# Optimization experiments

Measured on AMD Instinct MI355X. Metric: run time of the kernel, lower is better.

The kernel has to match this reference:

```python
import jax, jax.numpy as jnp
import numpy as np

IMG = 224; P = 16; C = 3
G = IMG // P; N = G * G            # 14, 196 patches
DIM = 768; DEPTH = 6; HEADS = 12; DH = 64; MLP = 3072
INNER = HEADS * DH                  # 768
PD = C * P * P                      # 768 patch_dim
B = 32


def _coords():
    m, n = np.meshgrid(np.arange(G), np.arange(G))
    return jnp.asarray(np.stack((m, n), axis=-1).reshape(-1, 2), jnp.float32)  # (N,2)


def _ln(x, g, b, eps=1e-5):
    mu = jnp.mean(x, -1, keepdims=True)
    var = jnp.mean((x - mu) ** 2, -1, keepdims=True)
    return (x - mu) * jax.lax.rsqrt(var + eps) * g + b


def setup_inputs() -> dict:
    key = jax.random.key(0)
    ks = jax.random.split(key, 16)
    s = 0.02
    inp = {
        "img": jax.random.normal(ks[0], (B, C, IMG, IMG), jnp.float32),
        "noise_token": jnp.zeros((1,), jnp.float32),
        "A_noise": jax.random.normal(ks[1], (B, 2, 2), jnp.float32),
        "b_noise": jax.random.normal(ks[2], (B, 2), jnp.float32),
        "A_mean": jnp.eye(2, dtype=jnp.float32),
        "b_mean": jnp.zeros((2,), jnp.float32),
        "A_std": jnp.zeros((2, 2), jnp.float32),   # variance_init=0.0
        "b_std": jnp.zeros((2,), jnp.float32),
        "band_width": jnp.asarray(1.0, jnp.float32),
        "Wp": jax.random.normal(ks[3], (PD, DIM), jnp.float32) * s,
        "bp": jnp.zeros((DIM,), jnp.float32),
        "ln1_g": jnp.ones((DEPTH, DIM), jnp.float32),
        "ln1_b": jnp.zeros((DEPTH, DIM), jnp.float32),
        "Wqkv": jax.random.normal(ks[4], (DEPTH, DIM, 3 * INNER), jnp.float32) * s,
        "Wout": jax.random.normal(ks[5], (DEPTH, INNER, DIM), jnp.float32) * s,
        "bout": jnp.zeros((DEPTH, DIM), jnp.float32),
        "ln2_g": jnp.ones((DEPTH, DIM), jnp.float32),
        "ln2_b": jnp.zeros((DEPTH, DIM), jnp.float32),
        "Wff1": jax.random.normal(ks[6], (DEPTH, DIM, MLP), jnp.float32) * s,
        "bff1": jnp.zeros((DEPTH, MLP), jnp.float32),
        "Wff2": jax.random.normal(ks[7], (DEPTH, MLP, DIM), jnp.float32) * s,
        "bff2": jnp.zeros((DEPTH, DIM), jnp.float32),
        "Wep": jax.random.normal(ks[8], (DIM, PD), jnp.float32) * s,
        "bep": jnp.zeros((PD,), jnp.float32),
    }
    return inp


def reference(img, noise_token, A_noise, b_noise, A_mean, b_mean, A_std, b_std,
              band_width, Wp, bp, ln1_g, ln1_b, Wqkv, Wout, bout,
              ln2_g, ln2_b, Wff1, bff1, Wff2, bff2, Wep, bep):
    del noise_token  # deleted in the original forward
    b = img.shape[0]
    X = _coords()  # (N,2) base patch grid coords, non-trainable buffer
    # patchify: b c (h p1) (w p2) -> b (h w) (p1 p2 c)
    x = img.reshape(b, C, G, P, G, P).transpose(0, 2, 4, 3, 5, 1).reshape(b, N, PD)
    x = x @ Wp + bp
    # stochastic affine transform of coordinates
    A = A_mean + jax.nn.softplus(A_std) * A_noise          # (b,2,2)
    bt = b_mean + jax.nn.softplus(b_std) * b_noise         # (b,2)
    Xt = jnp.einsum('pd,bdo->bpo', X, A) + bt[:, None, :]  # (b,N,2)
    # RBF attention scores: dots[b,i,j] = -||Xt[b,j] - X[i]||^2 / band_width
    diff = Xt[:, None, :, :] - X[None, :, None, :]         # (b,N,N,2)
    dots = -jnp.sum(diff ** 2, axis=-1) / band_width       # (b,N,N)
    attn = jax.nn.softmax(dots, axis=-1)                   # same for all heads/layers
    for l in range(DEPTH):
        y = _ln(x, ln1_g[l], ln1_b[l])
        qkv = y @ Wqkv[l]                                  # q,k unused (pos_only=True)
        v = qkv[..., 2 * INNER:].reshape(b, N, HEADS, DH).transpose(0, 2, 1, 3)
        o = jnp.einsum('bij,bhjd->bhid', attn, v)
        o = o.transpose(0, 2, 1, 3).reshape(b, N, INNER)
        x = o @ Wout[l] + bout[l]                          # NOTE: no residual on attention (matches source)
        h = _ln(x, ln2_g[l], ln2_b[l])
        h = jax.nn.gelu(h @ Wff1[l] + bff1[l], approximate=False) @ Wff2[l] + bff2[l]
        x = x + h
    x = x @ Wep + bep
    # un-patchify: b (h w) (p1 p2 c) -> b c (h p1) (w p2)
    out = x.reshape(b, G, G, P, P, C).transpose(0, 5, 1, 3, 2, 4).reshape(b, C, IMG, IMG)
    return out
```

## Files before the change

### kernel.cpp

```cpp
#include <hip/hip_runtime.h>
#include <hip/hip_bf16.h>
#include <math.h>

#define NTOK 196
#define KPAD 224
#define BATCH 32
#define ROWS (BATCH * NTOK)
#define DIMC 768
#define MLPD 3072

typedef __hip_bfloat16 bf16;
typedef short bf16x8 __attribute__((ext_vector_type(8)));
typedef float f32x4 __attribute__((ext_vector_type(4)));

__device__ __forceinline__ void gload16(const void* g, void* l) {
    __builtin_amdgcn_global_load_lds(
        (__attribute__((address_space(1))) void*)const_cast<void*>(g),
        (__attribute__((address_space(3))) void*)l, 16, 0, 0);
}

__device__ __forceinline__ float softplus_f(float x) {
    return fmaxf(x, 0.f) + log1pf(expf(-fabsf(x)));
}
__device__ __forceinline__ float gelu_f(float x) {
    return 0.5f * x * (1.f + erff(x * 0.70710678118654752f));
}
__device__ __forceinline__ float to_f(float x) { return x; }
__device__ __forceinline__ float to_f(bf16 x) { return __bfloat162float(x); }

__global__ __launch_bounds__(64) void attn_kernel(
    const float* __restrict__ A_noise, const float* __restrict__ b_noise,
    const float* __restrict__ A_mean,  const float* __restrict__ b_mean,
    const float* __restrict__ A_std,   const float* __restrict__ b_std,
    const float* __restrict__ bwp, bf16* __restrict__ attn)
{
    int bi = blockIdx.x;
    int b = bi / NTOK, i = bi % NTOK;
    int lane = threadIdx.x;
    float A00 = A_mean[0] + softplus_f(A_std[0]) * A_noise[b * 4 + 0];
    float A01 = A_mean[1] + softplus_f(A_std[1]) * A_noise[b * 4 + 1];
    float A10 = A_mean[2] + softplus_f(A_std[2]) * A_noise[b * 4 + 2];
    float A11 = A_mean[3] + softplus_f(A_std[3]) * A_noise[b * 4 + 3];
    float bt0 = b_mean[0] + softplus_f(b_std[0]) * b_noise[b * 2 + 0];
    float bt1 = b_mean[1] + softplus_f(b_std[1]) * b_noise[b * 2 + 1];
    float inv_bw = 1.f / bwp[0];
    float Xi0 = (float)(i % 14), Xi1 = (float)(i / 14);
    float d[4];
    float mx = -1e30f;
    #pragma unroll
    for (int r = 0; r < 4; ++r) {
        int j = lane + r * 64;
        if (j < NTOK) {
            float Xj0 = (float)(j % 14), Xj1 = (float)(j / 14);
            float t0 = Xj0 * A00 + Xj1 * A10 + bt0 - Xi0;
            float t1 = Xj0 * A01 + Xj1 * A11 + bt1 - Xi1;
            d[r] = -(t0 * t0 + t1 * t1) * inv_bw;
            mx = fmaxf(mx, d[r]);
        } else d[r] = -1e30f;
    }
    for (int off = 1; off < 64; off <<= 1) mx = fmaxf(mx, __shfl_xor(mx, off));
    float e[4]; float s = 0.f;
    #pragma unroll
    for (int r = 0; r < 4; ++r) {
        int j = lane + r * 64;
        e[r] = (j < NTOK) ? expf(d[r] - mx) : 0.f;
        s += e[r];
    }
    for (int off = 1; off < 64; off <<= 1) s += __shfl_xor(s, off);
    float inv = 1.f / s;
    bf16* row = attn + (long)bi * KPAD;
    #pragma unroll
    for (int r = 0; r < 4; ++r) {
        int j = lane + r * 64;
        if (j < KPAD) row[j] = __float2bfloat16(j < NTOK ? e[r] * inv : 0.f);
    }
}

__global__ __launch_bounds__(256) void patchify_kernel(
    const float* __restrict__ img, bf16* __restrict__ Xp)
{
    long idx = (long)blockIdx.x * 256 + threadIdx.x;
    if (idx >= (long)ROWS * DIMC) return;
    int pd = (int)(idx % DIMC); long r = idx / DIMC;
    int n = (int)(r % NTOK); int b = (int)(r / NTOK);
    int c = pd % 3; int pp = pd / 3; int p2 = pp % 16; int p1 = pp / 16;
    int gw = n % 14, gh = n / 14;
    int h = gh * 16 + p1, w = gw * 16 + p2;
    Xp[idx] = __float2bfloat16(img[(((long)b * 3 + c) * 224 + h) * 224 + w]);
}

__global__ __launch_bounds__(256) void unpatchify_kernel(
    const float* __restrict__ xe, float* __restrict__ out)
{
    long idx = (long)blockIdx.x * 256 + threadIdx.x;
    if (idx >= (long)BATCH * 3 * 224 * 224) return;
    int w = (int)(idx % 224); long r = idx / 224;
    int h = (int)(r % 224); r /= 224;
    int c = (int)(r % 3); int b = (int)(r / 3);
    int gh = h / 16, p1 = h % 16, gw = w / 16, p2 = w % 16;
    int n = gh * 14 + gw;
    int pd = (p1 * 16 + p2) * 3 + c;
    out[idx] = xe[((long)b * NTOK + n) * DIMC + pd];
}

__global__ __launch_bounds__(256) void ln_kernel(
    const float* __restrict__ x, const float* __restrict__ g,
    const float* __restrict__ bb, bf16* __restrict__ y)
{
    int row = blockIdx.x;
    const float* xr = x + (long)row * DIMC;
    bf16* yr = y + (long)row * DIMC;
    int t = threadIdx.x;
    float v0 = xr[t], v1 = xr[t + 256], v2 = xr[t + 512];
    float s = v0 + v1 + v2;
    float s2 = v0 * v0 + v1 * v1 + v2 * v2;
    for (int off = 32; off; off >>= 1) { s += __shfl_down(s, off); s2 += __shfl_down(s2, off); }
    __shared__ float ps[4], ps2[4];
    if ((t & 63) == 0) { ps[t >> 6] = s; ps2[t >> 6] = s2; }
    __syncthreads();
    float S = ps[0] + ps[1] + ps[2] + ps[3];
    float S2 = ps2[0] + ps2[1] + ps2[2] + ps2[3];
    float mean = S * (1.f / DIMC);
    float var = S2 * (1.f / DIMC) - mean * mean;
    float rs = rsqrtf(var + 1e-5f);
    yr[t]       = __float2bfloat16((v0 - mean) * rs * g[t]       + bb[t]);
    yr[t + 256] = __float2bfloat16((v1 - mean) * rs * g[t + 256] + bb[t + 256]);
    yr[t + 512] = __float2bfloat16((v2 - mean) * rs * g[t + 512] + bb[t + 512]);
}

template<typename TIN>
__global__ __launch_bounds__(256) void transpose_cvt(
    const TIN* __restrict__ in, bf16* __restrict__ out,
    int R, int C, int ldin, int ldout, int Rpad, long sIn, long sOut)
{
    __shared__ float tile[32][33];
    in  += (long)blockIdx.z * sIn;
    out += (long)blockIdx.z * sOut;
    int c0 = blockIdx.x * 32, r0 = blockIdx.y * 32;
    int tx = threadIdx.x & 31, ty = threadIdx.x >> 5;
    #pragma unroll
    for (int i = 0; i < 32; i += 8) {
        int r = r0 + ty + i, c = c0 + tx;
        float v = 0.f;
        if (r < R && c < C) v = to_f(in[(long)r * ldin + c]);
        tile[ty + i][tx] = v;
    }
    __syncthreads();
    #pragma unroll
    for (int i = 0; i < 32; i += 8) {
        int c = c0 + ty + i, r = r0 + tx;
        if (c < C && r < Rpad) out[(long)c * ldout + r] = __float2bfloat16(tile[tx][ty + i]);
    }
}

__global__ __launch_bounds__(256) void cvt_kernel(const float* __restrict__ in,
                                                  bf16* __restrict__ out, int n)
{
    int i = blockIdx.x * 256 + threadIdx.x;
    if (i < n) out[i] = __float2bfloat16(in[i]);
}

__global__ __launch_bounds__(256) void cvt_wv_kernel(const float* __restrict__ Wqkv,
                                                     bf16* __restrict__ out)
{
    long i = (long)blockIdx.x * 256 + threadIdx.x;
    if (i >= 6L * 768 * 768) return;
    int c = (int)(i % 768); long rl = i / 768;
    int r = (int)(rl % 768); int l = (int)(rl / 768);
    out[i] = __float2bfloat16(Wqkv[((long)l * 768 + r) * 2304 + 1536 + c]);
}

template<int BN, int ACT, int ACCUM, int OUTF32, int GUARDM>
__global__ __launch_bounds__(256) void gemm_bf16(
    const bf16* __restrict__ A, const bf16* __restrict__ Bt,
    const float* __restrict__ bias, void* __restrict__ Cv,
    int M, int K, int lda, int ldb, int ldc,
    long sA, long sB, long sC)
{
    constexpr int FN = BN / 32;
    constexpr int LPT = 2 + BN / 64;
    constexpr int BSTRIDE = BN * 32;
    constexpr int SMEM = (BN == 128) ? 49152 : 36864;
    __shared__ __align__(16) char smem[SMEM];
    bf16* As = (bf16*)smem;
    bf16* Bs = (bf16*)(smem + 3 * 8192);
    A  += (long)blockIdx.z * sA;
    Bt += (long)blockIdx.z * sB;
    const int nwg = gridDim.x * gridDim.y;
    const int id = blockIdx.x + gridDim.x * blockIdx.y;
    const int q8 = nwg >> 3, r8 = nwg & 7;
    const int xcd = id & 7, jj = id >> 3;
    const int v = (xcd < r8 ? xcd * (q8 + 1) : r8 * (q8 + 1) + (xcd - r8) * q8) + jj;
    const int bx = v % gridDim.x, by = v / gridDim.x;
    const int m0 = by * 128, n0 = bx * BN;
    const int t = threadIdx.x, wave = t >> 6, lane = t & 63;
    const int lrow = t >> 2;
    const int lcol = ((t & 3) ^ ((lrow >> 1) & 3)) * 8;
    const bf16* ag = A  + (long)(m0 + lrow) * lda + lcol;
    const bf16* bg = Bt + (long)(n0 + lrow) * ldb + lcol;
    const int fr = lane & 15, kq = lane >> 4;
    const int swz = (fr >> 1) & 3;
    const int wr = wave >> 1, wc = wave & 1;
    f32x4 acc[4][FN];
    #pragma unroll
    for (int m = 0; m < 4; ++m)
        #pragma unroll
        for (int n = 0; n < FN; ++n) acc[m][n] = (f32x4){0.f, 0.f, 0.f, 0.f};

    auto stage = [&](int kt, int bufi) {
        const int k0 = kt << 5;
        bf16* ab = As + bufi * 4096 + wave * 512;
        bf16* bb = Bs + bufi * BSTRIDE + wave * 512;
        gload16(ag + k0, ab);
        gload16(ag + 64 * (long)lda + k0, ab + 2048);
        gload16(bg + k0, bb);
        if constexpr (BN == 128) gload16(bg + 64 * (long)ldb + k0, bb + 2048);
    };
    auto compute = [&](int bufi) {
        const bf16* as = As + bufi * 4096;
        const bf16* bs = Bs + bufi * BSTRIDE;
        bf16x8 af[4], bfv[FN];
        #pragma unroll
        for (int m = 0; m < 4; ++m)
            af[m] = *(const bf16x8*)&as[(wr * 64 + m * 16 + fr) * 32 + ((kq ^ swz) << 3)];
        #pragma unroll
        for (int n = 0; n < FN; ++n)
            bfv[n] = *(const bf16x8*)&bs[(wc * (BN / 2) + n * 16 + fr) * 32 + ((kq ^ swz) << 3)];
        __builtin_amdgcn_s_setprio(1);
        #pragma unroll
        for (int m = 0; m < 4; ++m)
            #pragma unroll
            for (int n = 0; n < FN; ++n)
                acc[m][n] = __builtin_amdgcn_mfma_f32_16x16x32_bf16(af[m], bfv[n], acc[m][n], 0, 0, 0);
        __builtin_amdgcn_s_setprio(0);
    };

    const int nt = K >> 5;
    stage(0, 0);
    stage(1, 1);
    int cur = 0, pf = 2;
    for (int it = 0; it < nt - 1; ++it) {
        asm volatile("s_waitcnt vmcnt(%0)" :: "n"(LPT) : "memory");
        __builtin_amdgcn_s_barrier();
        __builtin_amdgcn_sched_barrier(0);
        if (it + 2 < nt) stage(it + 2, pf);
        compute(cur);
        cur = (cur == 2) ? 0 : cur + 1;
        pf  = (pf  == 2) ? 0 : pf + 1;
    }
    asm volatile("s_waitcnt vmcnt(0)" ::: "memory");
    __builtin_amdgcn_s_barrier();
    __builtin_amdgcn_sched_barrier(0);
    compute(cur);
    __syncthreads();

    const int rbase = kq * 4;
    if constexpr (OUTF32) {
        static_assert(BN == 64, "f32 epilogue assumes BN=64");
        float* Cs = (float*)smem;
        #pragma unroll
        for (int n = 0; n < FN; ++n) {
            int lc = wc * (BN / 2) + n * 16 + fr;
            float bi = bias ? bias[n0 + lc] : 0.f;
            #pragma unroll
            for (int m = 0; m < 4; ++m)
                #pragma unroll
                for (int r = 0; r < 4; ++r) {
                    int lr = wr * 64 + m * 16 + rbase + r;
                    float vv = acc[m][n][r] + bi;
                    if (ACT) vv = gelu_f(vv);
                    Cs[lr * BN + lc] = vv;
                }
        }
        __syncthreads();
        float* Cp = (float*)Cv + (long)blockIdx.z * sC;
        #pragma unroll
        for (int i = 0; i < (128 * BN) / (256 * 4); ++i) {
            int chunk = i * 256 + t;
            int row = chunk / (BN / 4), c4 = (chunk % (BN / 4)) * 4;
            int gm = m0 + row;
            if (GUARDM && gm >= M) continue;
            float4 v4 = *(const float4*)&Cs[row * BN + c4];
            float* p = Cp + (long)gm * ldc + n0 + c4;
            if (ACCUM) {
                float4 o4 = *(const float4*)p;
                v4.x += o4.x; v4.y += o4.y; v4.z += o4.z; v4.w += o4.w;
            }
            *(float4*)p = v4;
        }
    } else {
        bf16* Cs = (bf16*)smem;
        #pragma unroll
        for (int n = 0; n < FN; ++n) {
            int lc = wc * (BN / 2) + n * 16 + fr;
            float bi = bias ? bias[n0 + lc] : 0.f;
            #pragma unroll
            for (int m = 0; m < 4; ++m)
                #pragma unroll
                for (int r = 0; r < 4; ++r) {
                    int lr = wr * 64 + m * 16 + rbase + r;
                    float vv = acc[m][n][r] + bi;
                    if (ACT) vv = gelu_f(vv);
                    Cs[lr * BN + lc] = __float2bfloat16(vv);
                }
        }
        __syncthreads();
        bf16* Cp = (bf16*)Cv + (long)blockIdx.z * sC;
        #pragma unroll
        for (int i = 0; i < (128 * BN) / (256 * 8); ++i) {
            int chunk = i * 256 + t;
            int row = chunk / (BN / 8), c8 = (chunk % (BN / 8)) * 8;
            int gm = m0 + row;
            if (GUARDM && gm >= M) continue;
            *(bf16x8*)(Cp + (long)gm * ldc + n0 + c8) = *(const bf16x8*)&Cs[row * BN + c8];
        }
    }
}

extern "C" void kernel_launch(void* const* d_in, const int* in_sizes, int n_in,
                              void* d_out, int out_size, void* d_ws, size_t ws_size,
                              hipStream_t stream) {
    const float* img     = (const float*)d_in[0];
    const float* A_noise = (const float*)d_in[2];
    const float* b_noise = (const float*)d_in[3];
    const float* A_mean  = (const float*)d_in[4];
    const float* b_mean  = (const float*)d_in[5];
    const float* A_std   = (const float*)d_in[6];
    const float* b_std   = (const float*)d_in[7];
    const float* band_w  = (const float*)d_in[8];
    const float* Wp      = (const float*)d_in[9];
    const float* bp      = (const float*)d_in[10];
    const float* ln1_g   = (const float*)d_in[11];
    const float* ln1_b   = (const float*)d_in[12];
    const float* Wqkv    = (const float*)d_in[13];
    const float* Wout    = (const float*)d_in[14];
    const float* bout    = (const float*)d_in[15];
    const float* ln2_g   = (const float*)d_in[16];
    const float* ln2_b   = (const float*)d_in[17];
    const float* Wff1    = (const float*)d_in[18];
    const float* bff1    = (const float*)d_in[19];
    const float* Wff2    = (const float*)d_in[20];
    const float* bff2    = (const float*)d_in[21];
    const float* Wep     = (const float*)d_in[22];
    const float* bep     = (const float*)d_in[23];
    float* out = (float*)d_out;

    char* w = (char*)d_ws;
    bf16* WpT  = (bf16*)w; w += 768L * 768 * 2;
    bf16* WepT = (bf16*)w; w += 768L * 768 * 2;
    bf16* WvoT = (bf16*)w; w += 6L * 768 * 768 * 2;
    bf16* Wf1T = (bf16*)w; w += 6L * 3072 * 768 * 2;
    bf16* Wf2T = (bf16*)w; w += 6L * 768 * 3072 * 2;
    bf16* attnb = (bf16*)w; w += (long)(ROWS + 64) * KPAD * 2;
    bf16* Xpb  = (bf16*)w; w += (long)ROWS * DIMC * 2;
    bf16* yb   = (bf16*)w; w += (long)ROWS * DIMC * 2;
    bf16* yTb  = (bf16*)w; w += (long)BATCH * DIMC * KPAD * 2;
    bf16* ya   = (bf16*)w; w += (long)ROWS * DIMC * 2;
    bf16* h1b  = (bf16*)w; w += (long)ROWS * MLPD * 2;
    float* x   = (float*)w; w += (long)ROWS * DIMC * 4;
    bf16* WoT  = h1b;
    bf16* Wvb  = h1b + 6L * 768 * 768;

    transpose_cvt<float><<<dim3(24, 24, 1), 256, 0, stream>>>(Wp,  WpT,  768, 768, 768, 768, 768, 0, 0);
    transpose_cvt<float><<<dim3(24, 24, 1), 256, 0, stream>>>(Wep, WepT, 768, 768, 768, 768, 768, 0, 0);
    transpose_cvt<float><<<dim3(24, 24, 6), 256, 0, stream>>>(Wout, WoT, 768, 768, 768, 768, 768,
                                                              768L * 768, 768L * 768);
    cvt_wv_kernel<<<(int)((6L * 768 * 768 + 255) / 256), 256, 0, stream>>>(Wqkv, Wvb);
    transpose_cvt<float><<<dim3(96, 24, 6), 256, 0, stream>>>(Wff1, Wf1T, 768, 3072, 3072, 768, 768,
                                                              768L * 3072, 3072L * 768);
    transpose_cvt<float><<<dim3(24, 96, 6), 256, 0, stream>>>(Wff2, Wf2T, 3072, 768, 768, 3072, 3072,
                                                              3072L * 768, 768L * 3072);
    gemm_bf16<64, 0, 0, 0, 0><<<dim3(12, 6, 6), 256, 0, stream>>>(
        WoT, Wvb, nullptr, WvoT, 768, 768, 768, 768, 768,
        768L * 768, 768L * 768, 768L * 768);

    attn_kernel<<<ROWS, 64, 0, stream>>>(A_noise, b_noise, A_mean, b_mean, A_std, b_std, band_w, attnb);

    patchify_kernel<<<(ROWS * DIMC + 255) / 256, 256, 0, stream>>>(img, Xpb);
    gemm_bf16<64, 0, 0, 1, 0><<<dim3(12, 49, 1), 256, 0, stream>>>(
        Xpb, WpT, bp, x, ROWS, 768, 768, 768, 768, 0, 0, 0);

    for (int l = 0; l < 6; ++l) {
        ln_kernel<<<ROWS, 256, 0, stream>>>(x, ln1_g + l * 768, ln1_b + l * 768, yb);
        transpose_cvt<bf16><<<dim3(24, 7, 32), 256, 0, stream>>>(
            yb, yTb, NTOK, 768, 768, KPAD, KPAD, (long)NTOK * 768, (long)768 * KPAD);
        gemm_bf16<64, 0, 0, 0, 1><<<dim3(12, 2, BATCH), 256, 0, stream>>>(
            attnb, yTb, nullptr, ya, NTOK, KPAD, KPAD, KPAD, 768,
            (long)NTOK * KPAD, (long)768 * KPAD, (long)NTOK * 768);
        gemm_bf16<64, 0, 0, 1, 0><<<dim3(12, 49, 1), 256, 0, stream>>>(
            ya, WvoT + (long)l * 768 * 768, bout + l * 768, x, ROWS, 768, 768, 768, 768, 0, 0, 0);
        ln_kernel<<<ROWS, 256, 0, stream>>>(x, ln2_g + l * 768, ln2_b + l * 768, yb);
        gemm_bf16<64, 1, 0, 0, 0><<<dim3(48, 49, 1), 256, 0, stream>>>(
            yb, Wf1T + (long)l * 3072 * 768, bff1 + l * 3072, h1b, ROWS, 768, 768, 768, 3072, 0, 0, 0);
        gemm_bf16<64, 0, 1, 1, 0><<<dim3(12, 49, 1), 256, 0, stream>>>(
            h1b, Wf2T + (long)l * 768 * 3072, bff2 + l * 768, x, ROWS, 3072, 3072, 3072, 768, 0, 0, 0);
    }

    bf16* xb = Xpb;
    float* xe = (float*)h1b;
    cvt_kernel<<<(ROWS * DIMC + 255) / 256, 256, 0, stream>>>(x, xb, ROWS * DIMC);
    gemm_bf16<64, 0, 0, 1, 0><<<dim3(12, 49, 1), 256, 0, stream>>>(
        xb, WepT, bep, xe, ROWS, 768, 768, 768, 768, 0, 0, 0);
    unpatchify_kernel<<<(BATCH * 3 * 224 * 224 + 255) / 256, 256, 0, stream>>>(xe, out);
}
```

Measured before the change: 1.207 ms.

## Split-K the FF2 GEMM and fuse residual, bias and next LN into a combine kernel

The FF2 GEMM (K=3072) now runs as two K halves in one launch, each writing an fp32 partial buffer, which doubles the block count to fill more CUs. A new combine_ln kernel sums the residual, both partials and the bias, then applies the next layer's LN1 (or, in the last layer, just converts to bf16). That removes the separate LN1 launch per layer and the final cvt kernel. In exchange the GEMM writes and re-reads two fp32 partial buffers held in reused workspace, which adds memory traffic.

After: 1.180 ms. 1.02x faster.

```diff
diff --git a/kernel.cpp b/kernel.cpp
--- a/kernel.cpp
+++ b/kernel.cpp
@@ -128,6 +128,44 @@
     yr[t + 512] = __float2bfloat16((v2 - mean) * rs * g[t + 512] + bb[t + 512]);
 }
 
+template<int MODE>
+__global__ __launch_bounds__(256) void combine_ln(
+    const float* __restrict__ P0, const float* __restrict__ P1,
+    const float* __restrict__ bias, const float* __restrict__ x,
+    const float* __restrict__ g, const float* __restrict__ bb,
+    bf16* __restrict__ zb)
+{
+    int row = blockIdx.x;
+    const float* xr = x + (long)row * DIMC;
+    const float* p0 = P0 + (long)row * DIMC;
+    const float* p1 = P1 + (long)row * DIMC;
+    bf16* zr = zb + (long)row * DIMC;
+    int t = threadIdx.x;
+    float v0 = xr[t]       + p0[t]       + p1[t]       + bias[t];
+    float v1 = xr[t + 256] + p0[t + 256] + p1[t + 256] + bias[t + 256];
+    float v2 = xr[t + 512] + p0[t + 512] + p1[t + 512] + bias[t + 512];
+    if (MODE == 1) {
+        zr[t]       = __float2bfloat16(v0);
+        zr[t + 256] = __float2bfloat16(v1);
+        zr[t + 512] = __float2bfloat16(v2);
+        return;
+    }
+    float s = v0 + v1 + v2;
+    float s2 = v0 * v0 + v1 * v1 + v2 * v2;
+    for (int off = 32; off; off >>= 1) { s += __shfl_down(s, off); s2 += __shfl_down(s2, off); }
+    __shared__ float ps[4], ps2[4];
+    if ((t & 63) == 0) { ps[t >> 6] = s; ps2[t >> 6] = s2; }
+    __syncthreads();
+    float S = ps[0] + ps[1] + ps[2] + ps[3];
+    float S2 = ps2[0] + ps2[1] + ps2[2] + ps2[3];
+    float mean = S * (1.f / DIMC);
+    float var = S2 * (1.f / DIMC) - mean * mean;
+    float rs = rsqrtf(var + 1e-5f);
+    zr[t]       = __float2bfloat16((v0 - mean) * rs * g[t]       + bb[t]);
+    zr[t + 256] = __float2bfloat16((v1 - mean) * rs * g[t + 256] + bb[t + 256]);
+    zr[t + 512] = __float2bfloat16((v2 - mean) * rs * g[t + 512] + bb[t + 512]);
+}
+
 template<typename TIN>
 __global__ __launch_bounds__(256) void transpose_cvt(
     const TIN* __restrict__ in, bf16* __restrict__ out,
@@ -151,13 +189,6 @@
         int c = c0 + ty + i, r = r0 + tx;
         if (c < C && r < Rpad) out[(long)c * ldout + r] = __float2bfloat16(tile[tx][ty + i]);
     }
-}
-
-__global__ __launch_bounds__(256) void cvt_kernel(const float* __restrict__ in,
-                                                  bf16* __restrict__ out, int n)
-{
-    int i = blockIdx.x * 256 + threadIdx.x;
-    if (i < n) out[i] = __float2bfloat16(in[i]);
 }
 
 __global__ __launch_bounds__(256) void cvt_wv_kernel(const float* __restrict__ Wqkv,
@@ -358,8 +389,12 @@
     bf16* ya   = (bf16*)w; w += (long)ROWS * DIMC * 2;
     bf16* h1b  = (bf16*)w; w += (long)ROWS * MLPD * 2;
     float* x   = (float*)w; w += (long)ROWS * DIMC * 4;
-    bf16* WoT  = h1b;
-    bf16* Wvb  = h1b + 6L * 768 * 768;
+    float* P0 = (float*)Xpb;
+    float* P1 = P0 + (long)ROWS * DIMC;
+    bf16* WoT = h1b;
+    bf16* Wvb = h1b + 6L * 768 * 768;
+    bf16* zb  = h1b;
+    float* xe = (float*)((char*)h1b + (long)ROWS * DIMC * 2);
 
     transpose_cvt<float><<<dim3(24, 24, 1), 256, 0, stream>>>(Wp,  WpT,  768, 768, 768, 768, 768, 0, 0);
     transpose_cvt<float><<<dim3(24, 24, 1), 256, 0, stream>>>(Wep, WepT, 768, 768, 768, 768, 768, 0, 0);
@@ -379,11 +414,11 @@
     patchify_kernel<<<(ROWS * DIMC + 255) / 256, 256, 0, stream>>>(img, Xpb);
     gemm_bf16<64, 0, 0, 1, 0><<<dim3(12, 49, 1), 256, 0, stream>>>(
         Xpb, WpT, bp, x, ROWS, 768, 768, 768, 768, 0, 0, 0);
+    ln_kernel<<<ROWS, 256, 0, stream>>>(x, ln1_g, ln1_b, zb);
 
     for (int l = 0; l < 6; ++l) {
-        ln_kernel<<<ROWS, 256, 0, stream>>>(x, ln1_g + l * 768, ln1_b + l * 768, yb);
         transpose_cvt<bf16><<<dim3(24, 7, 32), 256, 0, stream>>>(
-            yb, yTb, NTOK, 768, 768, KPAD, KPAD, (long)NTOK * 768, (long)768 * KPAD);
+            zb, yTb, NTOK, 768, 768, KPAD, KPAD, (long)NTOK * 768, (long)768 * KPAD);
         gemm_bf16<64, 0, 0, 0, 1><<<dim3(12, 2, BATCH), 256, 0, stream>>>(
             attnb, yTb, nullptr, ya, NTOK, KPAD, KPAD, KPAD, 768,
             (long)NTOK * KPAD, (long)768 * KPAD, (long)NTOK * 768);
@@ -392,14 +427,18 @@
         ln_kernel<<<ROWS, 256, 0, stream>>>(x, ln2_g + l * 768, ln2_b + l * 768, yb);
         gemm_bf16<64, 1, 0, 0, 0><<<dim3(48, 49, 1), 256, 0, stream>>>(
             yb, Wf1T + (long)l * 3072 * 768, bff1 + l * 3072, h1b, ROWS, 768, 768, 768, 3072, 0, 0, 0);
-        gemm_bf16<64, 0, 1, 1, 0><<<dim3(12, 49, 1), 256, 0, stream>>>(
-            h1b, Wf2T + (long)l * 768 * 3072, bff2 + l * 768, x, ROWS, 3072, 3072, 3072, 768, 0, 0, 0);
-    }
-
-    bf16* xb = Xpb;
-    float* xe = (float*)h1b;
-    cvt_kernel<<<(ROWS * DIMC + 255) / 256, 256, 0, stream>>>(x, xb, ROWS * DIMC);
+        gemm_bf16<64, 0, 0, 1, 0><<<dim3(12, 49, 2), 256, 0, stream>>>(
+            h1b, Wf2T + (long)l * 768 * 3072, nullptr, P0,
+            ROWS, 1536, 3072, 3072, 768, 1536, 1536, (long)ROWS * DIMC);
+        if (l < 5)
+            combine_ln<0><<<ROWS, 256, 0, stream>>>(P0, P1, bff2 + l * 768, x,
+                ln1_g + (l + 1) * 768, ln1_b + (l + 1) * 768, zb);
+        else
+            combine_ln<1><<<ROWS, 256, 0, stream>>>(P0, P1, bff2 + l * 768, x,
+                ln1_g, ln1_b, zb);
+    }
+
     gemm_bf16<64, 0, 0, 1, 0><<<dim3(12, 49, 1), 256, 0, stream>>>(
-        xb, WepT, bep, xe, ROWS, 768, 768, 768, 768, 0, 0, 0);
+        zb, WepT, bep, xe, ROWS, 768, 768, 768, 768, 0, 0, 0);
     unpatchify_kernel<<<(BATCH * 3 * 224 * 224 + 255) / 256, 256, 0, stream>>>(xe, out);
 }
```
